# Performance work log

Hardware: AMD Instinct MI355X
Metric: run time of the kernel (lower is better)

## Reference

```python
import jax, jax.numpy as jnp
import numpy as np
import math

N = 8192
D = 512

def setup_inputs() -> dict:
    key = jax.random.key(0)
    k1, k2, k3, k4, k5 = jax.random.split(key, 5)
    x = jax.random.normal(k1, (N, D), dtype=jnp.float32)
    mask = jax.random.randint(k2, (N, N), 0, 2) == 1
    s = 1.0 / math.sqrt(D)
    Wq = jax.random.normal(k3, (D, D), dtype=jnp.float32) * s
    Wk = jax.random.normal(k4, (D, D), dtype=jnp.float32) * s
    Wv = jax.random.normal(k5, (D, D), dtype=jnp.float32) * s
    return {"x": x, "mask": mask, "Wq": Wq, "Wk": Wk, "Wv": Wv}

def reference(x, mask, Wq, Wk, Wv):
    d_model = x.shape[-1]
    # torch nn.Linear: y = x @ W^T
    Q = x @ Wq.T
    K = x @ Wk.T
    V = x @ Wv.T
    scores = (Q @ K.T) / jnp.sqrt(jnp.asarray(d_model, x.dtype))  # [N, N]
    scores = jnp.where(mask, jnp.asarray(-1e9, x.dtype), scores)
    # manual stable softmax, matching the original op sequence
    scores = jnp.exp(scores - jnp.max(scores, axis=1, keepdims=True))
    attn = scores / jnp.sum(scores, axis=-1, keepdims=True)
    cntx = attn @ V
    return (cntx, attn)
```

## Files before the change

### kernel.cpp

```cpp
#include <hip/hip_runtime.h>

#define NTOK 8192
#define DMODEL 512

typedef _Float16 f16;
typedef _Float16 f16x4 __attribute__((ext_vector_type(4)));
typedef _Float16 f16x8 __attribute__((ext_vector_type(8)));
typedef float f32x4 __attribute__((ext_vector_type(4)));

__device__ __forceinline__ void async_ld16(const void* g, void* l) {
  __builtin_amdgcn_global_load_lds((const __attribute__((address_space(1))) void*)g,
                                   (__attribute__((address_space(3))) void*)l, 16, 0, 0);
}

__global__ void pack_f16(const float* __restrict__ s, f16* __restrict__ d, int n) {
  int i = (blockIdx.x * 256 + threadIdx.x) * 4;
  if (i >= n) return;
  float4 v = *(const float4*)(s + i);
  f16x4 h; h.x = (f16)v.x; h.y = (f16)v.y; h.z = (f16)v.z; h.w = (f16)v.w;
  *(f16x4*)(d + i) = h;
}

__global__ __launch_bounds__(256) void transpose_f16(const f16* __restrict__ src,
                                                     f16* __restrict__ dst) {
  __shared__ f16 T[64][72];
  int t = threadIdx.x;
  int tok0 = blockIdx.x * 64, d0 = blockIdx.y * 64;
#pragma unroll
  for (int i = 0; i < 2; ++i) {
    int row = (t >> 3) + i * 32;
    int col = (t & 7) * 8;
    f16x8 v = *(const f16x8*)(src + (size_t)(tok0 + row) * DMODEL + d0 + col);
    *(f16x8*)(&T[row][col]) = v;
  }
  __syncthreads();
#pragma unroll
  for (int i = 0; i < 2; ++i) {
    int od = (t >> 3) + i * 32;
    int ot = (t & 7) * 8;
    f16x8 v;
#pragma unroll
    for (int j = 0; j < 8; ++j) v[j] = T[ot + j][od];
    *(f16x8*)(dst + (size_t)(d0 + od) * NTOK + tok0 + ot) = v;
  }
}

__device__ __forceinline__ void stage128x32(const f16* G, int r0, int k0, int rs,
                                            f16* lds, int t) {
  int wv = t >> 6;
  const f16* g0 = G + (size_t)(r0 + (t >> 2)) * rs + k0 + (t & 3) * 8;
  async_ld16(g0, (char*)lds + wv * 1024);
  const f16* g1 = g0 + (size_t)64 * rs;
  async_ld16(g1, (char*)lds + 4096 + wv * 1024);
}

__global__ __launch_bounds__(256) void qkv_gemm(const f16* __restrict__ X,
                                                const f16* __restrict__ Wall,
                                                f16* __restrict__ Out) {
  __shared__ f16 As[128 * 32];
  __shared__ f16 Bs[128 * 32];
  int t = threadIdx.x;
  int z = blockIdx.z;
  const f16* B = Wall + (size_t)z * DMODEL * DMODEL;
  f16* C = Out + (size_t)z * NTOK * DMODEL;
  int m0 = blockIdx.y * 128, n0 = blockIdx.x * 128;
  int lane = t & 63, wv = t >> 6, quad = lane >> 4, l15 = lane & 15;
  int m_off = (wv & 1) * 64, n_off = (wv >> 1) * 64;
  f32x4 acc[4][4] = {};
  for (int kt = 0; kt < DMODEL; kt += 32) {
    __syncthreads();
    stage128x32(X, m0, kt, DMODEL, As, t);
    stage128x32(B, n0, kt, DMODEL, Bs, t);
    __syncthreads();
    f16x8 af[4], bf[4];
    const f16x8* Av = (const f16x8*)As;
    const f16x8* Bv = (const f16x8*)Bs;
#pragma unroll
    for (int mt = 0; mt < 4; ++mt) af[mt] = Av[(m_off + mt * 16 + l15) * 4 + quad];
#pragma unroll
    for (int nt = 0; nt < 4; ++nt) bf[nt] = Bv[(n_off + nt * 16 + l15) * 4 + quad];
#pragma unroll
    for (int mt = 0; mt < 4; ++mt)
#pragma unroll
      for (int nt = 0; nt < 4; ++nt)
        acc[mt][nt] = __builtin_amdgcn_mfma_f32_16x16x32_f16(af[mt], bf[nt], acc[mt][nt], 0, 0, 0);
  }
#pragma unroll
  for (int mt = 0; mt < 4; ++mt)
#pragma unroll
    for (int nt = 0; nt < 4; ++nt)
#pragma unroll
      for (int r = 0; r < 4; ++r) {
        int row = m0 + m_off + mt * 16 + quad * 4 + r;
        int col = n0 + n_off + nt * 16 + l15;
        C[(size_t)row * DMODEL + col] = (f16)acc[mt][nt][r];
      }
}

__global__ __launch_bounds__(256) void scores_kernel(const f16* __restrict__ Q,
                                                     const f16* __restrict__ Kh,
                                                     const int* __restrict__ mask,
                                                     f16* __restrict__ E,
                                                     float* __restrict__ rowsum) {
  __shared__ f16 As[128 * 32];
  __shared__ f16 Bs[128 * 32];
  int t = threadIdx.x;
  int m0 = blockIdx.y * 128, n0 = blockIdx.x * 128;
  int lane = t & 63, wv = t >> 6, quad = lane >> 4, l15 = lane & 15;
  int m_off = (wv & 1) * 64, n_off = (wv >> 1) * 64;
  f32x4 acc[4][4] = {};
  for (int kt = 0; kt < DMODEL; kt += 32) {
    __syncthreads();
    stage128x32(Q, m0, kt, DMODEL, As, t);
    stage128x32(Kh, n0, kt, DMODEL, Bs, t);
    __syncthreads();
    f16x8 af[4], bf[4];
    const f16x8* Av = (const f16x8*)As;
    const f16x8* Bv = (const f16x8*)Bs;
#pragma unroll
    for (int mt = 0; mt < 4; ++mt) af[mt] = Av[(m_off + mt * 16 + l15) * 4 + quad];
#pragma unroll
    for (int nt = 0; nt < 4; ++nt) bf[nt] = Bv[(n_off + nt * 16 + l15) * 4 + quad];
#pragma unroll
    for (int mt = 0; mt < 4; ++mt)
#pragma unroll
      for (int nt = 0; nt < 4; ++nt)
        acc[mt][nt] = __builtin_amdgcn_mfma_f32_16x16x32_f16(af[mt], bf[nt], acc[mt][nt], 0, 0, 0);
  }
  const float scale = 0.044194173824159216f;
#pragma unroll
  for (int mt = 0; mt < 4; ++mt)
#pragma unroll
    for (int r = 0; r < 4; ++r) {
      int row = m0 + m_off + mt * 16 + quad * 4 + r;
      float rs = 0.f;
#pragma unroll
      for (int nt = 0; nt < 4; ++nt) {
        int col = n0 + n_off + nt * 16 + l15;
        size_t idx = (size_t)row * NTOK + col;
        float s = acc[mt][nt][r] * scale;
        float e = mask[idx] ? 0.f : __expf(s);
        E[idx] = (f16)e;
        rs += e;
      }
      rs += __shfl_xor(rs, 1);
      rs += __shfl_xor(rs, 2);
      rs += __shfl_xor(rs, 4);
      rs += __shfl_xor(rs, 8);
      if (l15 == 0) atomicAdd(&rowsum[row], rs);
    }
}

__global__ __launch_bounds__(512, 2) void ev_norm(const f16* __restrict__ E,
                                                  const float* __restrict__ rowsum,
                                                  const f16* __restrict__ Vt,
                                                  float* __restrict__ attn,
                                                  float* __restrict__ cntx) {
  __shared__ f16 Es[128 * 32];
  __shared__ f16 Vs[512 * 32];
  int t = threadIdx.x;
  int r0 = blockIdx.x * 128;
  int k0 = blockIdx.y * 1024;
  int lane = t & 63, wv = t >> 6, quad = lane >> 4, l15 = lane & 15;
  int m_off = (wv & 1) * 64, n_off = (wv >> 1) * 128;
  int srow = t >> 2, scol = (t & 3) * 8;
  float rinv = 1.f / rowsum[r0 + srow];
  f32x4 acc[4][8] = {};
  for (int kt = k0; kt < k0 + 1024; kt += 32) {
    __syncthreads();
    {
      size_t g = (size_t)(r0 + srow) * NTOK + kt + scol;
      f16x8 e = *(const f16x8*)(E + g);
      float a[8];
#pragma unroll
      for (int j = 0; j < 8; ++j) a[j] = (float)e[j] * rinv;
      float4 w0 = {a[0], a[1], a[2], a[3]};
      float4 w1 = {a[4], a[5], a[6], a[7]};
      *(float4*)(attn + g) = w0;
      *(float4*)(attn + g + 4) = w1;
      f16x8 h;
#pragma unroll
      for (int j = 0; j < 8; ++j) h[j] = (f16)a[j];
      *(f16x8*)(Es + srow * 32 + scol) = h;
    }
#pragma unroll
    for (int i = 0; i < 4; ++i) {
      const f16* g = Vt + (size_t)((i * 512 + t) >> 2) * NTOK + kt + (t & 3) * 8;
      async_ld16(g, (char*)Vs + i * 8192 + wv * 1024);
    }
    __syncthreads();
    f16x8 af[4], bf[8];
    const f16x8* Ev = (const f16x8*)Es;
    const f16x8* Vv = (const f16x8*)Vs;
#pragma unroll
    for (int mt = 0; mt < 4; ++mt) af[mt] = Ev[(m_off + mt * 16 + l15) * 4 + quad];
#pragma unroll
    for (int nt = 0; nt < 8; ++nt) bf[nt] = Vv[(n_off + nt * 16 + l15) * 4 + quad];
#pragma unroll
    for (int mt = 0; mt < 4; ++mt)
#pragma unroll
      for (int nt = 0; nt < 8; ++nt)
        acc[mt][nt] = __builtin_amdgcn_mfma_f32_16x16x32_f16(af[mt], bf[nt], acc[mt][nt], 0, 0, 0);
  }
#pragma unroll
  for (int mt = 0; mt < 4; ++mt)
#pragma unroll
    for (int nt = 0; nt < 8; ++nt)
#pragma unroll
      for (int r = 0; r < 4; ++r) {
        int row = r0 + m_off + mt * 16 + quad * 4 + r;
        int col = n_off + nt * 16 + l15;
        atomicAdd(&cntx[(size_t)row * DMODEL + col], acc[mt][nt][r]);
      }
}

extern "C" void kernel_launch(void* const* d_in, const int* in_sizes, int n_in,
                              void* d_out, int out_size, void* d_ws, size_t ws_size,
                              hipStream_t stream) {
  const float* x  = (const float*)d_in[0];
  const int* mask = (const int*)d_in[1];
  const float* Wq = (const float*)d_in[2];
  const float* Wk = (const float*)d_in[3];
  const float* Wv = (const float*)d_in[4];
  float* cntx = (float*)d_out;
  float* attn = (float*)d_out + (size_t)NTOK * DMODEL;

  f16* e16 = (f16*)d_ws;
  f16* xh  = e16;
  f16* Wh  = e16 + (size_t)NTOK * DMODEL;
  f16* QKV = e16 + (size_t)NTOK * NTOK;
  f16* Qh  = QKV;
  f16* Kh  = QKV + (size_t)NTOK * DMODEL;
  f16* Vh  = QKV + (size_t)2 * NTOK * DMODEL;
  f16* Vt  = QKV + (size_t)3 * NTOK * DMODEL;
  float* rowsum = (float*)(Vt + (size_t)NTOK * DMODEL);

  hipMemsetAsync(cntx, 0, (size_t)NTOK * DMODEL * sizeof(float), stream);
  hipMemsetAsync(rowsum, 0, NTOK * sizeof(float), stream);

  pack_f16<<<dim3(NTOK * DMODEL / 1024), 256, 0, stream>>>(x, xh, NTOK * DMODEL);
  pack_f16<<<dim3(DMODEL * DMODEL / 1024), 256, 0, stream>>>(Wq, Wh, DMODEL * DMODEL);
  pack_f16<<<dim3(DMODEL * DMODEL / 1024), 256, 0, stream>>>(Wk, Wh + DMODEL * DMODEL, DMODEL * DMODEL);
  pack_f16<<<dim3(DMODEL * DMODEL / 1024), 256, 0, stream>>>(Wv, Wh + 2 * DMODEL * DMODEL, DMODEL * DMODEL);

  qkv_gemm<<<dim3(DMODEL / 128, NTOK / 128, 3), 256, 0, stream>>>(xh, Wh, QKV);
  transpose_f16<<<dim3(NTOK / 64, DMODEL / 64), 256, 0, stream>>>(Vh, Vt);
  scores_kernel<<<dim3(NTOK / 128, NTOK / 128), 256, 0, stream>>>(Qh, Kh, mask, e16, rowsum);
  ev_norm<<<dim3(NTOK / 128, 8), 512, 0, stream>>>(e16, rowsum, Vt, attn, cntx);
}
```

Baseline: 838.3 us.

## Stage mask via async LDS loads, coalesce E stores, double-buffer ev_norm

```diff
diff --git a/kernel.cpp b/kernel.cpp
--- a/kernel.cpp
+++ b/kernel.cpp
@@ -97,22 +97,28 @@
       }
 }
 
-__global__ __launch_bounds__(256) void scores_kernel(const f16* __restrict__ Q,
-                                                     const f16* __restrict__ Kh,
-                                                     const int* __restrict__ mask,
-                                                     f16* __restrict__ E,
-                                                     float* __restrict__ rowsum) {
+__global__ __launch_bounds__(256, 2) void scores_kernel(const f16* __restrict__ Q,
+                                                        const f16* __restrict__ Kh,
+                                                        const int* __restrict__ mask,
+                                                        f16* __restrict__ E,
+                                                        float* __restrict__ rowsum) {
   __shared__ f16 As[128 * 32];
   __shared__ f16 Bs[128 * 32];
+  __shared__ int MM[128 * 128];
   int t = threadIdx.x;
   int m0 = blockIdx.y * 128, n0 = blockIdx.x * 128;
   int lane = t & 63, wv = t >> 6, quad = lane >> 4, l15 = lane & 15;
   int m_off = (wv & 1) * 64, n_off = (wv >> 1) * 64;
   f32x4 acc[4][4] = {};
-  for (int kt = 0; kt < DMODEL; kt += 32) {
+  for (int it = 0; it < 16; ++it) {
+    int kt = it * 32;
     __syncthreads();
     stage128x32(Q, m0, kt, DMODEL, As, t);
     stage128x32(Kh, n0, kt, DMODEL, Bs, t);
+    {
+      const int* g = mask + (size_t)(m0 + it * 8 + wv * 2 + (lane >> 5)) * NTOK + n0 + (lane & 31) * 4;
+      async_ld16(g, (char*)MM + it * 4096 + wv * 1024);
+    }
     __syncthreads();
     f16x8 af[4], bf[4];
     const f16x8* Av = (const f16x8*)As;
@@ -128,27 +134,63 @@
         acc[mt][nt] = __builtin_amdgcn_mfma_f32_16x16x32_f16(af[mt], bf[nt], acc[mt][nt], 0, 0, 0);
   }
   const float scale = 0.044194173824159216f;
+  int mreg[16];
 #pragma unroll
   for (int mt = 0; mt < 4; ++mt)
 #pragma unroll
     for (int r = 0; r < 4; ++r) {
-      int row = m0 + m_off + mt * 16 + quad * 4 + r;
-      float rs = 0.f;
+      int row_l = m_off + mt * 16 + quad * 4 + r;
 #pragma unroll
       for (int nt = 0; nt < 4; ++nt) {
-        int col = n0 + n_off + nt * 16 + l15;
-        size_t idx = (size_t)row * NTOK + col;
+        mreg[(mt * 4 + r)] = 0;
+      }
+    }
+  int mbits[4][4];
+#pragma unroll
+  for (int mt = 0; mt < 4; ++mt)
+#pragma unroll
+    for (int r = 0; r < 4; ++r) {
+      int row_l = m_off + mt * 16 + quad * 4 + r;
+      int b = 0;
+#pragma unroll
+      for (int nt = 0; nt < 4; ++nt) {
+        int col_l = n_off + nt * 16 + l15;
+        b |= (MM[row_l * 128 + col_l] ? 1 : 0) << nt;
+      }
+      mbits[mt][r] = b;
+    }
+  __syncthreads();
+  f16* el = (f16*)MM;
+#pragma unroll
+  for (int mt = 0; mt < 4; ++mt)
+#pragma unroll
+    for (int r = 0; r < 4; ++r) {
+      int row_l = m_off + mt * 16 + quad * 4 + r;
+      int b = mbits[mt][r];
+#pragma unroll
+      for (int nt = 0; nt < 4; ++nt) {
+        int col_l = n_off + nt * 16 + l15;
         float s = acc[mt][nt][r] * scale;
-        float e = mask[idx] ? 0.f : __expf(s);
-        E[idx] = (f16)e;
-        rs += e;
-      }
-      rs += __shfl_xor(rs, 1);
-      rs += __shfl_xor(rs, 2);
-      rs += __shfl_xor(rs, 4);
-      rs += __shfl_xor(rs, 8);
-      if (l15 == 0) atomicAdd(&rowsum[row], rs);
+        float e = (b >> nt & 1) ? 0.f : __expf(s);
+        el[row_l * 128 + col_l] = (f16)e;
+      }
     }
+  __syncthreads();
+#pragma unroll
+  for (int itr = 0; itr < 8; ++itr) {
+    int row = itr * 16 + (t >> 4);
+    int col = (t & 15) * 8;
+    f16x8 v = *(const f16x8*)(el + row * 128 + col);
+    *(f16x8*)(E + (size_t)(m0 + row) * NTOK + n0 + col) = v;
+    float s8 = 0.f;
+#pragma unroll
+    for (int j = 0; j < 8; ++j) s8 += (float)v[j];
+    s8 += __shfl_xor(s8, 1);
+    s8 += __shfl_xor(s8, 2);
+    s8 += __shfl_xor(s8, 4);
+    s8 += __shfl_xor(s8, 8);
+    if (l15 == 0) atomicAdd(&rowsum[m0 + row], s8);
+  }
 }
 
 __global__ __launch_bounds__(512, 2) void ev_norm(const f16* __restrict__ E,
@@ -156,42 +198,58 @@
                                                   const f16* __restrict__ Vt,
                                                   float* __restrict__ attn,
                                                   float* __restrict__ cntx) {
-  __shared__ f16 Es[128 * 32];
-  __shared__ f16 Vs[512 * 32];
+  __shared__ f16 Es[2][128 * 32];
+  __shared__ f16 Vs[2][512 * 32];
   int t = threadIdx.x;
   int r0 = blockIdx.x * 128;
-  int k0 = blockIdx.y * 1024;
+  int k0 = blockIdx.y * 2048;
+  int kend = k0 + 2048;
   int lane = t & 63, wv = t >> 6, quad = lane >> 4, l15 = lane & 15;
   int m_off = (wv & 1) * 64, n_off = (wv >> 1) * 128;
   int srow = t >> 2, scol = (t & 3) * 8;
+  size_t erow = (size_t)(r0 + srow) * NTOK;
   float rinv = 1.f / rowsum[r0 + srow];
   f32x4 acc[4][8] = {};
-  for (int kt = k0; kt < k0 + 1024; kt += 32) {
-    __syncthreads();
-    {
-      size_t g = (size_t)(r0 + srow) * NTOK + kt + scol;
-      f16x8 e = *(const f16x8*)(E + g);
-      float a[8];
-#pragma unroll
-      for (int j = 0; j < 8; ++j) a[j] = (float)e[j] * rinv;
-      float4 w0 = {a[0], a[1], a[2], a[3]};
-      float4 w1 = {a[4], a[5], a[6], a[7]};
-      *(float4*)(attn + g) = w0;
-      *(float4*)(attn + g + 4) = w1;
-      f16x8 h;
-#pragma unroll
-      for (int j = 0; j < 8; ++j) h[j] = (f16)a[j];
-      *(f16x8*)(Es + srow * 32 + scol) = h;
-    }
-#pragma unroll
-    for (int i = 0; i < 4; ++i) {
-      const f16* g = Vt + (size_t)((i * 512 + t) >> 2) * NTOK + kt + (t & 3) * 8;
-      async_ld16(g, (char*)Vs + i * 8192 + wv * 1024);
-    }
-    __syncthreads();
+
+#define STAGE_V(KT, BUF)                                                              \
+  {                                                                                   \
+    _Pragma("unroll") for (int i = 0; i < 4; ++i) {                                   \
+      const f16* g = Vt + (size_t)(i * 128 + (t >> 2)) * NTOK + (KT) + (t & 3) * 8;   \
+      async_ld16(g, (char*)&Vs[BUF][0] + i * 8192 + wv * 1024);                       \
+    }                                                                                 \
+  }
+
+#define PROCESS_E(EREG, KT, BUF)                                                      \
+  {                                                                                   \
+    float a[8];                                                                       \
+    _Pragma("unroll") for (int j = 0; j < 8; ++j) a[j] = (float)(EREG)[j] * rinv;     \
+    float4 w0 = {a[0], a[1], a[2], a[3]};                                             \
+    float4 w1 = {a[4], a[5], a[6], a[7]};                                             \
+    *(float4*)(attn + erow + (KT) + scol) = w0;                                       \
+    *(float4*)(attn + erow + (KT) + scol + 4) = w1;                                   \
+    f16x8 h;                                                                          \
+    _Pragma("unroll") for (int j = 0; j < 8; ++j) h[j] = (f16)a[j];                   \
+    *(f16x8*)(&Es[BUF][srow * 32 + scol]) = h;                                        \
+  }
+
+  f16x8 eA = *(const f16x8*)(E + erow + k0 + scol);
+  STAGE_V(k0, 0);
+  PROCESS_E(eA, k0, 0);
+  f16x8 eB = *(const f16x8*)(E + erow + k0 + 32 + scol);
+  int cur = 0;
+
+  for (int kt = k0; kt < kend; kt += 32) {
+    __syncthreads();
+    int nxt = cur ^ 1;
+    bool more = (kt + 32) < kend;
+    bool more2 = (kt + 64) < kend;
+    if (more) STAGE_V(kt + 32, nxt);
+    f16x8 eC = eB;
+    if (more2) eC = *(const f16x8*)(E + erow + kt + 64 + scol);
+    if (more) PROCESS_E(eB, kt + 32, nxt);
     f16x8 af[4], bf[8];
-    const f16x8* Ev = (const f16x8*)Es;
-    const f16x8* Vv = (const f16x8*)Vs;
+    const f16x8* Ev = (const f16x8*)&Es[cur][0];
+    const f16x8* Vv = (const f16x8*)&Vs[cur][0];
 #pragma unroll
     for (int mt = 0; mt < 4; ++mt) af[mt] = Ev[(m_off + mt * 16 + l15) * 4 + quad];
 #pragma unroll
@@ -201,6 +259,8 @@
 #pragma unroll
       for (int nt = 0; nt < 8; ++nt)
         acc[mt][nt] = __builtin_amdgcn_mfma_f32_16x16x32_f16(af[mt], bf[nt], acc[mt][nt], 0, 0, 0);
+    eB = eC;
+    cur = nxt;
   }
 #pragma unroll
   for (int mt = 0; mt < 4; ++mt)
@@ -212,6 +272,8 @@
         int col = n_off + nt * 16 + l15;
         atomicAdd(&cntx[(size_t)row * DMODEL + col], acc[mt][nt][r]);
       }
+#undef STAGE_V
+#undef PROCESS_E
 }
 
 extern "C" void kernel_launch(void* const* d_in, const int* in_sizes, int n_in,
@@ -246,5 +308,5 @@
   qkv_gemm<<<dim3(DMODEL / 128, NTOK / 128, 3), 256, 0, stream>>>(xh, Wh, QKV);
   transpose_f16<<<dim3(NTOK / 64, DMODEL / 64), 256, 0, stream>>>(Vh, Vt);
   scores_kernel<<<dim3(NTOK / 128, NTOK / 128), 256, 0, stream>>>(Qh, Kh, mask, e16, rowsum);
-  ev_norm<<<dim3(NTOK / 128, 8), 512, 0, stream>>>(e16, rowsum, Vt, attn, cntx);
-}
+  ev_norm<<<dim3(NTOK / 128, 4), 512, 0, stream>>>(e16, rowsum, Vt, attn, cntx);
+}
```

New measurement: 837.5 us. Within noise of the previous version (-0.1%).
